# Kernel optimization log

Hardware: AMD Instinct MI355X
Metric: run time of the kernel (lower is better)

Reference implementation:

```python
import jax, jax.numpy as jnp
import numpy as np

B, N, A = 2, 4096, 5
TOPK = 30
K_RBF = 16
MAX_AA = 22
MAXREL = 32
EDGE_IN = 16 + K_RBF * 25 + 14 + 16  # 446
EDGE_FEAT = 128
PI = 3.1415926


def l2norm(v, eps=1e-12):
    n = jnp.sqrt(jnp.sum(v * v, axis=-1, keepdims=True))
    return v / jnp.maximum(n, eps)


def gather_nodes(nodes, idx):
    # nodes: (B,N,C), idx: (B,N,K) -> (B,N,K,C)
    b, n, k = idx.shape
    flat = idx.reshape(b, n * k, 1)
    out = jnp.take_along_axis(nodes, flat, axis=1)
    return out.reshape(b, n, k, nodes.shape[-1])


def quaternions(R):
    # R: (...,3,3) -> unit quaternion (...,4)
    Rxx, Ryy, Rzz = R[..., 0, 0], R[..., 1, 1], R[..., 2, 2]
    mag = 0.5 * jnp.sqrt(jnp.abs(1.0 + jnp.stack([Rxx - Ryy - Rzz, -Rxx + Ryy - Rzz, -Rxx - Ryy + Rzz], -1)) + 1e-12)
    signs = jnp.sign(jnp.stack([R[..., 2, 1] - R[..., 1, 2], R[..., 0, 2] - R[..., 2, 0], R[..., 1, 0] - R[..., 0, 1]], -1))
    xyz = signs * mag
    w = jnp.sqrt(jax.nn.relu(1.0 + Rxx + Ryy + Rzz) + 1e-12)[..., None] / 2.0
    return l2norm(jnp.concatenate([xyz, w], -1))


def setup_inputs():
    key = jax.random.key(0)
    ks = jax.random.split(key, 12)
    X = jax.random.normal(ks[0], (B, N, A, 3), jnp.float32) * 3.0
    mask = jnp.ones((B, N), jnp.float32)
    mask_atoms = jnp.ones((B, N, A), jnp.float32)
    means = jax.random.normal(ks[1], (K_RBF,), jnp.float32)
    stds = jax.random.normal(ks[2], (K_RBF,), jnp.float32)
    mul_w = jax.random.normal(ks[3], (A * A,), jnp.float32)
    bias_w = jax.random.normal(ks[4], (A * A,), jnp.float32)
    aa_pair_embed = jax.random.normal(ks[5], (MAX_AA * MAX_AA, K_RBF), jnp.float32) * 0.02
    aa_pair_embed = aa_pair_embed.at[441].set(0.0)  # padding_idx
    relpos_embed = jax.random.normal(ks[6], (2 * MAXREL + 1, 16), jnp.float32) * 0.02
    mask_embed = jax.random.normal(ks[7], (2, 16), jnp.float32) * 0.02
    W1 = jax.random.normal(ks[8], (EDGE_IN, EDGE_IN), jnp.float32) / np.sqrt(EDGE_IN)
    b1 = jnp.zeros((EDGE_IN,), jnp.float32)
    W2 = jax.random.normal(ks[9], (EDGE_IN, EDGE_FEAT), jnp.float32) / np.sqrt(EDGE_IN)
    b2 = jnp.zeros((EDGE_FEAT,), jnp.float32)
    aa = jax.random.randint(ks[10], (B, N), 0, 21, jnp.int32)
    residue_idx = jnp.tile(jnp.arange(N, dtype=jnp.int32)[None, :], (B, 1))
    chain_labels = jax.random.randint(ks[11], (B, N), 0, 2, jnp.int32)
    return dict(X=X, mask=mask, mask_atoms=mask_atoms, means=means, stds=stds, mul_w=mul_w,
                bias_w=bias_w, aa_pair_embed=aa_pair_embed, relpos_embed=relpos_embed,
                mask_embed=mask_embed, W1=W1, b1=b1, W2=W2, b2=b2, aa=aa,
                residue_idx=residue_idx, chain_labels=chain_labels)


def reference(X, mask, mask_atoms, means, stds, mul_w, bias_w, aa_pair_embed, relpos_embed,
              mask_embed, W1, b1, W2, b2, aa, residue_idx, chain_labels):
    Ca = X[:, :, 1]  # (B,N,3) C-alpha
    # ---- _dist: spatial kNN over C-alpha ----
    mask2d = mask[:, :, None] * mask[:, None, :]
    dx = Ca[:, None, :, :] - Ca[:, :, None, :]
    D = mask2d * jnp.sqrt(jnp.sum(dx * dx, -1) + 1e-6)
    D_adj = D + (1.0 - mask2d) * jnp.max(D, -1, keepdims=True)
    _, E_idx = jax.lax.top_k(-D_adj, TOPK)  # smallest distances
    mask_attend = jnp.take_along_axis(mask2d, E_idx, axis=2)  # (B,N,K)
    # ---- orientation features (local frames + quaternions) ----
    ones3 = jnp.ones((B, 1, 3), X.dtype)
    u = l2norm(jnp.concatenate([ones3, Ca[:, 1:] - Ca[:, :-1]], 1))
    b_ = l2norm(jnp.concatenate([u[:, :-1] - u[:, 1:], ones3], 1))
    n_ = l2norm(jnp.concatenate([jnp.cross(u[:, :-1], u[:, 1:]), ones3], 1))
    lf = jnp.stack([b_, n_, jnp.cross(b_, n_)], axis=2)  # (B,N,3,3)
    X_nb = gather_nodes(Ca, E_idx)                       # (B,N,K,3)
    O_nb = gather_nodes(lf.reshape(B, N, 9), E_idx).reshape(B, N, TOPK, 3, 3)
    t = X_nb - Ca[:, :, None, :]
    t = jnp.einsum('bnij,bnkj->bnki', lf, t)
    t = l2norm(t) * mask_attend[..., None]
    r = jnp.einsum('bnji,bnkjl->bnkil', lf, O_nb)  # lf^T @ O_nb
    q = quaternions(r) * mask_attend[..., None]
    O_feat = jnp.concatenate([t, q, 1.0 - 2.0 * jnp.abs(t), 1.0 - 2.0 * jnp.abs(q)], -1)  # (B,N,K,14)
    # ---- positional / chain embeddings ----
    offset = residue_idx[:, :, None] - residue_idx[:, None, :]
    offset_nb = jnp.take_along_axis(offset, E_idx, 2)
    d_chain = (chain_labels[:, :, None] == chain_labels[:, None, :]).astype(jnp.int32)
    E_chains = jnp.take_along_axis(d_chain, E_idx, 2)
    d = jnp.clip(offset_nb + MAXREL, 0, 2 * MAXREL)
    E_pos = relpos_embed[d] + mask_embed[E_chains]  # (B,N,K,16)
    # ---- GaussianLayer: aa-pair embed + atom-pair distance RBF ----
    aa_pair = aa[:, :, None] * MAX_AA + aa[:, None, :]
    aa_nb = jnp.take_along_axis(aa_pair, E_idx, 2)
    feat_aapair = aa_pair_embed[aa_nb] * mask_attend[..., None]  # (B,N,K,16)
    nbX = gather_nodes(X.reshape(B, N, A * 3), E_idx).reshape(B, N, TOPK, A, 3)
    delta = nbX[:, :, :, :, None, :] - X[:, :, None, None, :, :]  # (B,N,K,A,A,3)
    Dab = jnp.sqrt(jnp.sum(delta * delta, -1) + 1e-12)            # (B,N,K,A,A)
    et = jnp.arange(A * A).reshape(A, A)
    xg = mul_w[et] * Dab + bias_w[et]
    m_nb = gather_nodes(mask_atoms, E_idx)  # (B,N,K,A)
    xg = xg * (m_nb[..., None, :] * m_nb[..., :, None])
    std = jnp.abs(stds) + 0.01
    g = jnp.exp(-0.5 * ((xg[..., None] - means) / std) ** 2) / ((2.0 * PI) ** 0.5 * std)
    gbf = g.reshape(B, N, TOPK, A * A * K_RBF) * mask_attend[..., None]  # (B,N,K,400)
    # ---- fuse and project (NonLinear gbf_proj) ----
    E = jnp.concatenate([E_pos, gbf, O_feat, feat_aapair], -1)  # (B,N,K,446)
    h = jax.nn.gelu(E @ W1 + b1, approximate=False)
    return h @ W2 + b2  # (B,N,K,128)
```

## Files before the change

kernel.cpp:

```cpp
#include <hip/hip_runtime.h>
#include <cstdint>
#include <cstddef>

#define NN 4096
#define TOPK_ 30
#define BN_TOT 8192
#define M_TOT 245760
#define KP 448
#define HSTRIDE 136
#define EF 128

typedef unsigned short u16;
typedef unsigned int u32;
typedef __attribute__((ext_vector_type(8))) short bf16x8;
typedef __attribute__((ext_vector_type(4))) float f32x4;

__device__ __forceinline__ float b2f(u16 u){ return __uint_as_float(((u32)u)<<16); }
__device__ __forceinline__ u16 f2b(float f){
  u32 u = __float_as_uint(f);
  return (u16)((u + 0x7FFFu + ((u>>16)&1u)) >> 16);
}
__device__ __forceinline__ float ldf(const void* p, long i, int fl){
  return fl ? ((const float*)p)[i] : b2f(((const u16*)p)[i]);
}
__device__ __forceinline__ int is_f32_flag(const u16* mask){
  return (((const u32*)mask)[0] == 0x3F800000u) ? 1 : 0;
}
__device__ __forceinline__ void norm3(float x,float y,float z,float&ox,float&oy,float&oz){
  float n = sqrtf(x*x+y*y+z*z); n = fmaxf(n, 1e-12f);
  ox=x/n; oy=y/n; oz=z/n;
}
__device__ __forceinline__ float sgn(float x){ return x>0.f?1.f:(x<0.f?-1.f:0.f); }
__device__ __forceinline__ float gelu_f(float x){
  return 0.5f*x*(1.0f + erff(x*0.70710678118654752440f));
}
__device__ __forceinline__ float gelu_fast(float x){
  float y = 0.70710678118654752440f * x;
  float s = fabsf(y);
  float t = __builtin_amdgcn_rcpf(fmaf(0.3275911f, s, 1.0f));
  float p = fmaf(fmaf(fmaf(fmaf(1.061405429f, t, -1.453152027f), t, 1.421413741f), t,
                 -0.284496736f), t, 0.254829592f);
  float e = __expf(-y*y);
  float erfs = fmaf(-p*t, e, 1.0f);
  float erfy = (x >= 0.f) ? erfs : -erfs;
  float hx = 0.5f*x;
  return fmaf(hx, erfy, hx);
}
__device__ __forceinline__ u32 pk_bf16(float lo, float hi){
  u32 r;
  asm("v_cvt_pk_bf16_f32 %0, %1, %2" : "=v"(r) : "v"(lo), "v"(hi));
  return r;
}
__device__ __forceinline__ void async_cp16(const void* g, void* l){
  __builtin_amdgcn_global_load_lds((const __attribute__((address_space(1))) void*)(uintptr_t)g,
                                   (__attribute__((address_space(3))) void*)(uintptr_t)l, 16, 0, 0);
}

__global__ __launch_bounds__(256) void prep_kernel(
    const void* __restrict__ X, const u16* __restrict__ mask,
    const void* __restrict__ W1, const void* __restrict__ b1,
    const void* __restrict__ W2, const void* __restrict__ b2,
    float* __restrict__ ca, float* __restrict__ lf,
    u16* __restrict__ W1P, u16* __restrict__ W2P,
    float* __restrict__ b1p, float* __restrict__ b2p)
{
  const int fl = is_f32_flag(mask);
  int idx = blockIdx.x*256 + threadIdx.x;
  if (idx < BN_TOT) {
    int i = idx & (NN-1);
    float cax = ldf(X, (long)idx*15+3, fl), cay = ldf(X, (long)idx*15+4, fl), caz = ldf(X, (long)idx*15+5, fl);
    ca[idx*4+0]=cax; ca[idx*4+1]=cay; ca[idx*4+2]=caz; ca[idx*4+3]=0.f;
    float bx,by,bz,nx,ny,nz;
    if (i < NN-1) {
      float uix,uiy,uiz;
      if (i==0) { norm3(1.f,1.f,1.f,uix,uiy,uiz); }
      else {
        float px=ldf(X,(long)(idx-1)*15+3,fl), py=ldf(X,(long)(idx-1)*15+4,fl), pz=ldf(X,(long)(idx-1)*15+5,fl);
        norm3(cax-px, cay-py, caz-pz, uix,uiy,uiz);
      }
      float qx=ldf(X,(long)(idx+1)*15+3,fl), qy=ldf(X,(long)(idx+1)*15+4,fl), qz=ldf(X,(long)(idx+1)*15+5,fl);
      float vx,vy,vz; norm3(qx-cax, qy-cay, qz-caz, vx,vy,vz);
      norm3(uix-vx, uiy-vy, uiz-vz, bx,by,bz);
      norm3(uiy*vz-uiz*vy, uiz*vx-uix*vz, uix*vy-uiy*vx, nx,ny,nz);
    } else {
      norm3(1.f,1.f,1.f,bx,by,bz); nx=bx; ny=by; nz=bz;
    }
    float cx = by*nz - bz*ny, cy = bz*nx - bx*nz, cz = bx*ny - by*nx;
    float* L = lf + (size_t)idx*12;
    L[0]=bx;L[1]=by;L[2]=bz;L[3]=nx;L[4]=ny;L[5]=nz;L[6]=cx;L[7]=cy;L[8]=cz;
    return;
  }
  int r1 = idx - BN_TOT;
  if (r1 < 229376) {
    int f = r1 >> 9, li = r1 & 511;
    int n0 = f / 14, kc = f - n0*14;
    int ln = li >> 3, j = li & 7;
    int n = n0*16 + (ln & 15);
    int k = kc*32 + (ln >> 4)*8 + j;
    W1P[r1] = (n < 446 && k < 446) ? (fl ? f2b(((const float*)W1)[(long)k*446 + n])
                                         : ((const u16*)W1)[(long)k*446 + n]) : (u16)0;
    return;
  }
  int r2 = r1 - 229376;
  if (r2 < 65536) {
    int f = r2 >> 9, li = r2 & 511;
    int n0 = f >> 4, kc = f & 15;
    int ln = li >> 3, j = li & 7;
    int n = n0*16 + (ln & 15);
    int k = kc*32 + (ln >> 4)*8 + j;
    W2P[r2] = (k < 446) ? (fl ? f2b(((const float*)W2)[(long)k*128 + n])
                              : ((const u16*)W2)[(long)k*128 + n]) : (u16)0;
    return;
  }
  int r3 = r2 - 65536;
  if (r3 < 512) { b1p[r3] = (r3<446)? ldf(b1, r3, fl) : 0.f; return; }
  int r4 = r3 - 512;
  if (r4 < 128) { b2p[r4] = ldf(b2, r4, fl); }
}

__global__ __launch_bounds__(64) void knn_kernel(const float4* __restrict__ ca,
                                                 int* __restrict__ eidx)
{
#pragma clang fp contract(off)
  __shared__ u32 keys[NN];
  int bi = blockIdx.x;
  int lane = threadIdx.x;
  int b = bi >> 12;
  const float4 ci = ca[bi];
  const float4* cab = ca + (b<<12);
  u32 mind = 0xFFFFFFFFu; int minj = 1<<30; int minslot = 0;
  for (int c = 0; c < 64; ++c) {
    int j = (c<<6) | lane;
    float4 cj = cab[j];
    float dx = cj.x-ci.x, dy = cj.y-ci.y, dz = cj.z-ci.z;
    float ss = dx*dx;
    ss = ss + dy*dy;
    ss = ss + dz*dz;
    float d = sqrtf(ss + 1e-6f);
    u32 db = __float_as_uint(d);
    keys[(c<<6)|lane] = db;
    if (db < mind) { mind = db; minj = j; minslot = c; }
  }
  __syncthreads();
  for (int r = 0; r < TOPK_; ++r) {
    u32 wd = mind; int wj = minj;
    #pragma unroll
    for (int off = 32; off; off >>= 1) {
      u32 od = __shfl_xor(wd, off, 64);
      int oj = __shfl_xor(wj, off, 64);
      if (od < wd || (od == wd && oj < wj)) { wd = od; wj = oj; }
    }
    if (lane == 0) eidx[bi*TOPK_ + r] = wj;
    if ((wj & 63) == lane && wj == minj) {
      keys[minslot*64 + lane] = 0xFFFFFFFFu;
      mind = 0xFFFFFFFFu; minj = 1<<30;
      for (int c = 0; c < 64; ++c) {
        u32 db = keys[(c<<6)|lane];
        if (db < mind) { mind = db; minj = (c<<6)|lane; minslot = c; }
      }
    }
  }
}

__global__ __launch_bounds__(256) void ofeat_kernel(
  const u16* __restrict__ mask, const float* __restrict__ ca, const float* __restrict__ lf,
  const int* __restrict__ eidx, u16* __restrict__ E, int chunkStart, int Mc)
{
  int t = blockIdx.x*256 + threadIdx.x;
  if (t >= Mc) return;
  long e = chunkStart + t;
  const int fl = is_f32_flag(mask);
  int k = (int)(e % TOPK_);
  long bi = e / TOPK_;
  int b = (int)(bi >> 12);
  int bj = (b<<12) + eidx[bi*TOPK_ + k];
  float ma = ldf(mask, bi, fl) * ldf(mask, bj, fl);
  float Li[9], Lj[9];
  #pragma unroll
  for (int q_ = 0; q_ < 9; ++q_) { Li[q_] = lf[(size_t)bi*12+q_]; Lj[q_] = lf[(size_t)bj*12+q_]; }
  float dx = ca[bj*4+0]-ca[bi*4+0], dy = ca[bj*4+1]-ca[bi*4+1], dz = ca[bj*4+2]-ca[bi*4+2];
  float t0 = Li[0]*dx+Li[1]*dy+Li[2]*dz;
  float t1 = Li[3]*dx+Li[4]*dy+Li[5]*dz;
  float t2 = Li[6]*dx+Li[7]*dy+Li[8]*dz;
  float tn = fmaxf(sqrtf(t0*t0+t1*t1+t2*t2), 1e-12f);
  t0 = t0/tn*ma; t1 = t1/tn*ma; t2 = t2/tn*ma;
  float R00=Li[0]*Lj[0]+Li[3]*Lj[3]+Li[6]*Lj[6];
  float R01=Li[0]*Lj[1]+Li[3]*Lj[4]+Li[6]*Lj[7];
  float R02=Li[0]*Lj[2]+Li[3]*Lj[5]+Li[6]*Lj[8];
  float R10=Li[1]*Lj[0]+Li[4]*Lj[3]+Li[7]*Lj[6];
  float R11=Li[1]*Lj[1]+Li[4]*Lj[4]+Li[7]*Lj[7];
  float R12=Li[1]*Lj[2]+Li[4]*Lj[5]+Li[7]*Lj[8];
  float R20=Li[2]*Lj[0]+Li[5]*Lj[3]+Li[8]*Lj[6];
  float R21=Li[2]*Lj[1]+Li[5]*Lj[4]+Li[8]*Lj[7];
  float R22=Li[2]*Lj[2]+Li[5]*Lj[5]+Li[8]*Lj[8];
  float m0 = 0.5f*sqrtf(fabsf(1.f+R00-R11-R22)+1e-12f);
  float m1 = 0.5f*sqrtf(fabsf(1.f-R00+R11-R22)+1e-12f);
  float m2 = 0.5f*sqrtf(fabsf(1.f-R00-R11+R22)+1e-12f);
  float q0 = sgn(R21-R12)*m0, q1 = sgn(R02-R20)*m1, q2 = sgn(R10-R01)*m2;
  float qw = 0.5f*sqrtf(fmaxf(1.f+R00+R11+R22, 0.f)+1e-12f);
  float qn = fmaxf(sqrtf(q0*q0+q1*q1+q2*q2+qw*qw), 1e-12f);
  q0 = q0/qn*ma; q1 = q1/qn*ma; q2 = q2/qn*ma; qw = qw/qn*ma;
  u16 vals[14];
  vals[0]=f2b(t0); vals[1]=f2b(t1); vals[2]=f2b(t2);
  vals[3]=f2b(q0); vals[4]=f2b(q1); vals[5]=f2b(q2); vals[6]=f2b(qw);
  vals[7]=f2b(1.f-2.f*fabsf(t0)); vals[8]=f2b(1.f-2.f*fabsf(t1)); vals[9]=f2b(1.f-2.f*fabsf(t2));
  vals[10]=f2b(1.f-2.f*fabsf(q0)); vals[11]=f2b(1.f-2.f*fabsf(q1));
  vals[12]=f2b(1.f-2.f*fabsf(q2)); vals[13]=f2b(1.f-2.f*fabsf(qw));
  u16* dst = E + (size_t)t*KP + 416;
  *(uint4*)dst = *(const uint4*)vals;
  *(uint2*)(dst+8) = *(const uint2*)(vals+8);
  *(u32*)(dst+12) = *(const u32*)(vals+12);
}

__global__ __launch_bounds__(256) void feat_kernel(
  const void* __restrict__ X, const u16* __restrict__ mask, const void* __restrict__ mask_atoms,
  const void* __restrict__ means, const void* __restrict__ stds,
  const void* __restrict__ mul_w, const void* __restrict__ bias_w,
  const void* __restrict__ aa_pe, const void* __restrict__ relpos, const void* __restrict__ mask_emb,
  const int* __restrict__ aa, const int* __restrict__ ridx, const int* __restrict__ chains,
  const int* __restrict__ eidx, u16* __restrict__ E, int chunkStart, int Mc)
{
  const int fl = is_f32_flag(mask);
  int lane = threadIdx.x & 63;
  long gw = (long)(blockIdx.x*4) + (threadIdx.x >> 6);
  long nw = (long)gridDim.x * 4;
  float stdv = fabsf(ldf(stds, lane & 15, fl)) + 0.01f;
  float rinv = 1.0f/stdv;
  float coef0 = 0.3989422804014327f*rinv;
  float rmean = ldf(means, lane & 15, fl);
  float mw = 0.f, bw = 0.f;
  if (lane < 25) { mw = ldf(mul_w, lane, fl); bw = ldf(bias_w, lane, fl); }
  for (long e = chunkStart + gw; e < chunkStart + Mc; e += nw) {
    int k = (int)(e % TOPK_);
    long bi = e / TOPK_;
    int b = (int)(bi >> 12);
    int bj = (b<<12) + eidx[bi*TOPK_ + k];
    float ma = ldf(mask, bi, fl) * ldf(mask, bj, fl);
    float xgv = 0.f;
    if (lane < 25) {
      int a = lane/5, c_ = lane - a*5;
      float d0 = ldf(X,(long)bj*15 + a*3+0,fl) - ldf(X,(long)bi*15 + c_*3+0,fl);
      float d1 = ldf(X,(long)bj*15 + a*3+1,fl) - ldf(X,(long)bi*15 + c_*3+1,fl);
      float d2 = ldf(X,(long)bj*15 + a*3+2,fl) - ldf(X,(long)bi*15 + c_*3+2,fl);
      float Dab = sqrtf(d0*d0 + d1*d1 + d2*d2 + 1e-12f);
      float mm = ldf(mask_atoms,(long)bj*5 + a,fl) * ldf(mask_atoms,(long)bj*5 + c_,fl);
      xgv = (mw*Dab + bw) * mm;
    }
    int d = ridx[bi] - ridx[bj] + 32; d = d < 0 ? 0 : (d > 64 ? 64 : d);
    int ch = (chains[bi] == chains[bj]) ? 1 : 0;
    int aap = aa[bi]*22 + aa[bj];
    u16* row = E + (size_t)(e - chunkStart) * KP;
    #pragma unroll
    for (int pass = 0; pass < 7; ++pass) {
      int f = pass*64 + lane;
      int p = (f - 16) >> 4;
      p = p < 0 ? 0 : (p > 24 ? 24 : p);
      float xv = __shfl(xgv, p, 64);
      float val; bool skip = false;
      if (f < 16) {
        val = ldf(relpos, d*16 + f, fl) + ldf(mask_emb, ch*16 + f, fl);
      } else if (f < 416) {
        float z = (xv - rmean) * rinv;
        val = __expf(-0.5f*z*z) * coef0 * ma;
      } else if (f < 430) {
        skip = true; val = 0.f;
      } else if (f < 446) {
        val = ldf(aa_pe, aap*16 + (f-430), fl) * ma;
      } else {
        val = 0.f;
      }
      if (!skip) row[f] = f2b(val);
    }
  }
}

__global__ __launch_bounds__(512,2) void fused_mlp(
    const u16* __restrict__ E, const u16* __restrict__ W1P, const u16* __restrict__ W2P,
    const float* __restrict__ b1p, const float* __restrict__ b2p,
    void* __restrict__ C, long outOff, const u16* maskp)
{
  __shared__ u16 smem[2*128*HSTRIDE];
  u16* hs0 = smem;
  u16* hs1 = smem + 128*HSTRIDE;
  int tid = threadIdx.x;
  int lane = tid & 63, wave = tid >> 6;
  int wr = wave >> 2, wc = wave & 3;
  long rowBase = (long)blockIdx.x * 128;

  #define STAGE(tt, buf) do {                                                     \
    int r0_ = tid >> 3, s0_ = tid & 7;                                            \
    async_cp16(E + (rowBase + r0_)*(long)KP + (tt)*64 + ((s0_ ^ (r0_ & 7))<<3),   \
               smem + (buf)*8192 + tid*8);                                        \
    int r1_ = 64 + r0_;                                                           \
    async_cp16(E + (rowBase + r1_)*(long)KP + (tt)*64 + ((s0_ ^ (r1_ & 7))<<3),   \
               smem + (buf)*8192 + 4096 + tid*8);                                 \
  } while(0)

  f32x4 acc1[4][4][2] = {};
  STAGE(0, 0);
  #pragma unroll 1
  for (int t = 0; t < 7; ++t) {
    __syncthreads();
    const u16* As = smem + (t&1)*8192;
    bf16x8 af[2][4];
    #pragma unroll
    for (int kk = 0; kk < 2; ++kk)
      #pragma unroll
      for (int r = 0; r < 4; ++r) {
        int row = wr*64 + r*16 + (lane&15);
        int s = kk*4 + (lane>>4);
        af[kk][r] = *(const bf16x8*)(As + row*64 + ((s ^ (row&7))<<3));
      }
    bf16x8 bgA[2][2][2];
    #pragma unroll
    for (int c = 0; c < 2; ++c)
      #pragma unroll
      for (int cc = 0; cc < 2; ++cc)
        #pragma unroll
        for (int kk = 0; kk < 2; ++kk)
          bgA[c][cc][kk] = *(const bf16x8*)(W1P + (((c*8 + wc*2 + cc)*14 + t*2 + kk) << 9) + lane*8);
    #pragma unroll
    for (int c = 0; c < 2; ++c)
      #pragma unroll
      for (int r = 0; r < 4; ++r)
        #pragma unroll
        for (int cc = 0; cc < 2; ++cc)
          #pragma unroll
          for (int kk = 0; kk < 2; ++kk)
            acc1[c][r][cc] = __builtin_amdgcn_mfma_f32_16x16x32_bf16(af[kk][r], bgA[c][cc][kk], acc1[c][r][cc], 0,0,0);
    bf16x8 bgB[2][2][2];
    #pragma unroll
    for (int c = 0; c < 2; ++c)
      #pragma unroll
      for (int cc = 0; cc < 2; ++cc)
        #pragma unroll
        for (int kk = 0; kk < 2; ++kk)
          bgB[c][cc][kk] = *(const bf16x8*)(W1P + ((((c+2)*8 + wc*2 + cc)*14 + t*2 + kk) << 9) + lane*8);
    __builtin_amdgcn_sched_barrier(0);
    if (t < 6) STAGE(t+1, (t+1)&1);
    __builtin_amdgcn_sched_barrier(0);
    #pragma unroll
    for (int c = 0; c < 2; ++c)
      #pragma unroll
      for (int r = 0; r < 4; ++r)
        #pragma unroll
        for (int cc = 0; cc < 2; ++cc)
          #pragma unroll
          for (int kk = 0; kk < 2; ++kk)
            acc1[c+2][r][cc] = __builtin_amdgcn_mfma_f32_16x16x32_bf16(af[kk][r], bgB[c][cc][kk], acc1[c+2][r][cc], 0,0,0);
  }
  #undef STAGE

  #define STORE_HS(cN, buf) do {                                                  \
    _Pragma("unroll")                                                             \
    for (int r = 0; r < 4; ++r) {                                                 \
      _Pragma("unroll")                                                           \
      for (int cc = 0; cc < 2; ++cc) {                                            \
        int col = wc*32 + cc*16 + (lane & 15);                                    \
        float bv = b1p[(cN)*128 + col];                                           \
        int row0 = wr*64 + r*16 + (lane>>4)*4;                                    \
        u32 p01 = pk_bf16(gelu_fast(acc1[cN][r][cc][0]+bv),                       \
                          gelu_fast(acc1[cN][r][cc][1]+bv));                      \
        u32 p23 = pk_bf16(gelu_fast(acc1[cN][r][cc][2]+bv),                       \
                          gelu_fast(acc1[cN][r][cc][3]+bv));                      \
        u16* hb_ = (buf) + row0*HSTRIDE + col;                                    \
        hb_[0]         = (u16)p01; hb_[HSTRIDE]   = (u16)(p01>>16);               \
        hb_[2*HSTRIDE] = (u16)p23; hb_[3*HSTRIDE] = (u16)(p23>>16);               \
      }                                                                           \
    }                                                                             \
  } while(0)

  f32x4 acc2[4][2] = {};
  __syncthreads();
  STORE_HS(0, hs0);
  __syncthreads();
  #pragma unroll
  for (int c = 0; c < 4; ++c) {
    u16* hb = (c & 1) ? hs1 : hs0;
    u16* hn = (c & 1) ? hs0 : hs1;
    if (c < 3) STORE_HS(c+1, hn);
    #pragma unroll
    for (int k2 = 0; k2 < 4; ++k2) {
      bf16x8 af2[4], bg2[2];
      #pragma unroll
      for (int r = 0; r < 4; ++r) {
        int row = wr*64 + r*16 + (lane&15);
        af2[r] = *(const bf16x8*)(hb + row*HSTRIDE + k2*32 + (lane>>4)*8);
      }
      #pragma unroll
      for (int cc = 0; cc < 2; ++cc)
        bg2[cc] = *(const bf16x8*)(W2P + ((((wc*2+cc)*16) + c*4 + k2) << 9) + lane*8);
      #pragma unroll
      for (int r = 0; r < 4; ++r)
        #pragma unroll
        for (int cc = 0; cc < 2; ++cc)
          acc2[r][cc] = __builtin_amdgcn_mfma_f32_16x16x32_bf16(af2[r], bg2[cc], acc2[r][cc], 0,0,0);
    }
    __syncthreads();
  }
  #undef STORE_HS

  const int f32out = is_f32_flag(maskp);
  #pragma unroll
  for (int r = 0; r < 4; ++r) {
    #pragma unroll
    for (int cc = 0; cc < 2; ++cc) {
      int col = wc*32 + cc*16 + (lane & 15);
      float bv = b2p[col];
      #pragma unroll
      for (int g = 0; g < 4; ++g) {
        long row = rowBase + wr*64 + r*16 + (lane>>4)*4 + g;
        float v = acc2[r][cc][g] + bv;
        long o = outOff + row*EF + col;
        if (f32out) ((float*)C)[o] = v;
        else        ((u16*)C)[o]  = f2b(v);
      }
    }
  }
}

extern "C" void kernel_launch(void* const* d_in, const int* in_sizes, int n_in,
                              void* d_out, int out_size, void* d_ws, size_t ws_size,
                              hipStream_t stream) {
  const void* X          = d_in[0];
  const u16* mask        = (const u16*)d_in[1];
  const void* mask_atoms = d_in[2];
  const void* means      = d_in[3];
  const void* stds       = d_in[4];
  const void* mul_w      = d_in[5];
  const void* bias_w     = d_in[6];
  const void* aa_pe      = d_in[7];
  const void* relpos     = d_in[8];
  const void* mask_emb   = d_in[9];
  const void* W1         = d_in[10];
  const void* b1         = d_in[11];
  const void* W2         = d_in[12];
  const void* b2         = d_in[13];
  const int* aa          = (const int*)d_in[14];
  const int* ridx        = (const int*)d_in[15];
  const int* chains      = (const int*)d_in[16];

  char* ws = (char*)d_ws;
  float* ca  = (float*)(ws + 0);
  float* lf  = (float*)(ws + 131072);
  int* eidx  = (int*)(ws + 524288);
  u16* W1P   = (u16*)(ws + 1507328);
  u16* W2P   = (u16*)(ws + 1966080);
  float* b1p = (float*)(ws + 2097152);
  float* b2p = (float*)(ws + 2099200);
  size_t base = 2099712;

  int nc = 64;
  for (int c = 1; c <= 64; c <<= 1) {
    size_t mc = (size_t)M_TOT / c;
    if (base + mc*896 <= ws_size) { nc = c; break; }
  }
  int Mc = M_TOT / nc;
  u16* Ebuf = (u16*)(ws + base);

  prep_kernel<<<1187, 256, 0, stream>>>(X, mask, W1, b1, W2, b2, ca, lf, W1P, W2P, b1p, b2p);
  knn_kernel<<<BN_TOT, 64, 0, stream>>>((const float4*)ca, eidx);
  for (int c = 0; c < nc; ++c) {
    int cs = c * Mc;
    feat_kernel<<<1024, 256, 0, stream>>>(X, mask, mask_atoms, means, stds, mul_w, bias_w,
                                          aa_pe, relpos, mask_emb, aa, ridx, chains,
                                          eidx, Ebuf, cs, Mc);
    ofeat_kernel<<<Mc/256, 256, 0, stream>>>(mask, ca, lf, eidx, Ebuf, cs, Mc);
    fused_mlp<<<Mc/128, 512, 0, stream>>>(Ebuf, W1P, W2P, b1p, b2p, d_out,
                                          (long)cs*EF, mask);
  }
}
```

Before: 785.1 us.

## Fuse edge feature generation into MLP kernel, build E tile in LDS

Merges the feature kernels (relpos, RBF, orientation, aa-pair) into the MLP kernel. Each block now computes its 128-row, 448-column bf16 feature tile directly into swizzled LDS instead of writing a large E buffer to global memory and reading it back with async copies. This removes the chunk loop, the extra launches and the global round trip of roughly 220MB of intermediate data. In exchange, LDS use per block grows to about 118KB, which may cut occupancy below the two blocks per CU the launch bounds ask for. The pipelined staging of the A tiles is also gone, so each block does all its feature math before its first MFMA.

```diff
diff --git a/kernel.cpp b/kernel.cpp
--- a/kernel.cpp
+++ b/kernel.cpp
@@ -31,9 +31,6 @@
   ox=x/n; oy=y/n; oz=z/n;
 }
 __device__ __forceinline__ float sgn(float x){ return x>0.f?1.f:(x<0.f?-1.f:0.f); }
-__device__ __forceinline__ float gelu_f(float x){
-  return 0.5f*x*(1.0f + erff(x*0.70710678118654752440f));
-}
 __device__ __forceinline__ float gelu_fast(float x){
   float y = 0.70710678118654752440f * x;
   float s = fabsf(y);
@@ -50,10 +47,6 @@
   u32 r;
   asm("v_cvt_pk_bf16_f32 %0, %1, %2" : "=v"(r) : "v"(lo), "v"(hi));
   return r;
-}
-__device__ __forceinline__ void async_cp16(const void* g, void* l){
-  __builtin_amdgcn_global_load_lds((const __attribute__((address_space(1))) void*)(uintptr_t)g,
-                                   (__attribute__((address_space(3))) void*)(uintptr_t)l, 16, 0, 0);
 }
 
 __global__ __launch_bounds__(256) void prep_kernel(
@@ -162,146 +155,168 @@
   }
 }
 
-__global__ __launch_bounds__(256) void ofeat_kernel(
-  const u16* __restrict__ mask, const float* __restrict__ ca, const float* __restrict__ lf,
-  const int* __restrict__ eidx, u16* __restrict__ E, int chunkStart, int Mc)
+__global__ __launch_bounds__(512,2) void mega_mlp(
+    const void* __restrict__ X, const u16* __restrict__ mask, const void* __restrict__ mask_atoms,
+    const void* __restrict__ means, const void* __restrict__ stds,
+    const void* __restrict__ mul_w, const void* __restrict__ bias_w,
+    const void* __restrict__ aa_pe, const void* __restrict__ relpos, const void* __restrict__ mask_emb,
+    const int* __restrict__ aa, const int* __restrict__ ridx, const int* __restrict__ chains,
+    const int* __restrict__ eidx, const float* __restrict__ ca, const float* __restrict__ lf,
+    const u16* __restrict__ W1P, const u16* __restrict__ W2P,
+    const float* __restrict__ b1p, const float* __restrict__ b2p,
+    void* __restrict__ C)
 {
-  int t = blockIdx.x*256 + threadIdx.x;
-  if (t >= Mc) return;
-  long e = chunkStart + t;
+  __shared__ __align__(16) u16 Et[128*448];
+  __shared__ float Dabs[128][29];
+  __shared__ float maA[128];
   const int fl = is_f32_flag(mask);
-  int k = (int)(e % TOPK_);
-  long bi = e / TOPK_;
-  int b = (int)(bi >> 12);
-  int bj = (b<<12) + eidx[bi*TOPK_ + k];
-  float ma = ldf(mask, bi, fl) * ldf(mask, bj, fl);
-  float Li[9], Lj[9];
-  #pragma unroll
-  for (int q_ = 0; q_ < 9; ++q_) { Li[q_] = lf[(size_t)bi*12+q_]; Lj[q_] = lf[(size_t)bj*12+q_]; }
-  float dx = ca[bj*4+0]-ca[bi*4+0], dy = ca[bj*4+1]-ca[bi*4+1], dz = ca[bj*4+2]-ca[bi*4+2];
-  float t0 = Li[0]*dx+Li[1]*dy+Li[2]*dz;
-  float t1 = Li[3]*dx+Li[4]*dy+Li[5]*dz;
-  float t2 = Li[6]*dx+Li[7]*dy+Li[8]*dz;
-  float tn = fmaxf(sqrtf(t0*t0+t1*t1+t2*t2), 1e-12f);
-  t0 = t0/tn*ma; t1 = t1/tn*ma; t2 = t2/tn*ma;
-  float R00=Li[0]*Lj[0]+Li[3]*Lj[3]+Li[6]*Lj[6];
-  float R01=Li[0]*Lj[1]+Li[3]*Lj[4]+Li[6]*Lj[7];
-  float R02=Li[0]*Lj[2]+Li[3]*Lj[5]+Li[6]*Lj[8];
-  float R10=Li[1]*Lj[0]+Li[4]*Lj[3]+Li[7]*Lj[6];
-  float R11=Li[1]*Lj[1]+Li[4]*Lj[4]+Li[7]*Lj[7];
-  float R12=Li[1]*Lj[2]+Li[4]*Lj[5]+Li[7]*Lj[8];
-  float R20=Li[2]*Lj[0]+Li[5]*Lj[3]+Li[8]*Lj[6];
-  float R21=Li[2]*Lj[1]+Li[5]*Lj[4]+Li[8]*Lj[7];
-  float R22=Li[2]*Lj[2]+Li[5]*Lj[5]+Li[8]*Lj[8];
-  float m0 = 0.5f*sqrtf(fabsf(1.f+R00-R11-R22)+1e-12f);
-  float m1 = 0.5f*sqrtf(fabsf(1.f-R00+R11-R22)+1e-12f);
-  float m2 = 0.5f*sqrtf(fabsf(1.f-R00-R11+R22)+1e-12f);
-  float q0 = sgn(R21-R12)*m0, q1 = sgn(R02-R20)*m1, q2 = sgn(R10-R01)*m2;
-  float qw = 0.5f*sqrtf(fmaxf(1.f+R00+R11+R22, 0.f)+1e-12f);
-  float qn = fmaxf(sqrtf(q0*q0+q1*q1+q2*q2+qw*qw), 1e-12f);
-  q0 = q0/qn*ma; q1 = q1/qn*ma; q2 = q2/qn*ma; qw = qw/qn*ma;
-  u16 vals[14];
-  vals[0]=f2b(t0); vals[1]=f2b(t1); vals[2]=f2b(t2);
-  vals[3]=f2b(q0); vals[4]=f2b(q1); vals[5]=f2b(q2); vals[6]=f2b(qw);
-  vals[7]=f2b(1.f-2.f*fabsf(t0)); vals[8]=f2b(1.f-2.f*fabsf(t1)); vals[9]=f2b(1.f-2.f*fabsf(t2));
-  vals[10]=f2b(1.f-2.f*fabsf(q0)); vals[11]=f2b(1.f-2.f*fabsf(q1));
-  vals[12]=f2b(1.f-2.f*fabsf(q2)); vals[13]=f2b(1.f-2.f*fabsf(qw));
-  u16* dst = E + (size_t)t*KP + 416;
-  *(uint4*)dst = *(const uint4*)vals;
-  *(uint2*)(dst+8) = *(const uint2*)(vals+8);
-  *(u32*)(dst+12) = *(const u32*)(vals+12);
-}
-
-__global__ __launch_bounds__(256) void feat_kernel(
-  const void* __restrict__ X, const u16* __restrict__ mask, const void* __restrict__ mask_atoms,
-  const void* __restrict__ means, const void* __restrict__ stds,
-  const void* __restrict__ mul_w, const void* __restrict__ bias_w,
-  const void* __restrict__ aa_pe, const void* __restrict__ relpos, const void* __restrict__ mask_emb,
-  const int* __restrict__ aa, const int* __restrict__ ridx, const int* __restrict__ chains,
-  const int* __restrict__ eidx, u16* __restrict__ E, int chunkStart, int Mc)
-{
-  const int fl = is_f32_flag(mask);
-  int lane = threadIdx.x & 63;
-  long gw = (long)(blockIdx.x*4) + (threadIdx.x >> 6);
-  long nw = (long)gridDim.x * 4;
-  float stdv = fabsf(ldf(stds, lane & 15, fl)) + 0.01f;
-  float rinv = 1.0f/stdv;
-  float coef0 = 0.3989422804014327f*rinv;
-  float rmean = ldf(means, lane & 15, fl);
-  float mw = 0.f, bw = 0.f;
-  if (lane < 25) { mw = ldf(mul_w, lane, fl); bw = ldf(bias_w, lane, fl); }
-  for (long e = chunkStart + gw; e < chunkStart + Mc; e += nw) {
-    int k = (int)(e % TOPK_);
-    long bi = e / TOPK_;
-    int b = (int)(bi >> 12);
-    int bj = (b<<12) + eidx[bi*TOPK_ + k];
-    float ma = ldf(mask, bi, fl) * ldf(mask, bj, fl);
-    float xgv = 0.f;
-    if (lane < 25) {
-      int a = lane/5, c_ = lane - a*5;
-      float d0 = ldf(X,(long)bj*15 + a*3+0,fl) - ldf(X,(long)bi*15 + c_*3+0,fl);
-      float d1 = ldf(X,(long)bj*15 + a*3+1,fl) - ldf(X,(long)bi*15 + c_*3+1,fl);
-      float d2 = ldf(X,(long)bj*15 + a*3+2,fl) - ldf(X,(long)bi*15 + c_*3+2,fl);
-      float Dab = sqrtf(d0*d0 + d1*d1 + d2*d2 + 1e-12f);
-      float mm = ldf(mask_atoms,(long)bj*5 + a,fl) * ldf(mask_atoms,(long)bj*5 + c_,fl);
-      xgv = (mw*Dab + bw) * mm;
-    }
-    int d = ridx[bi] - ridx[bj] + 32; d = d < 0 ? 0 : (d > 64 ? 64 : d);
-    int ch = (chains[bi] == chains[bj]) ? 1 : 0;
-    int aap = aa[bi]*22 + aa[bj];
-    u16* row = E + (size_t)(e - chunkStart) * KP;
-    #pragma unroll
-    for (int pass = 0; pass < 7; ++pass) {
-      int f = pass*64 + lane;
-      int p = (f - 16) >> 4;
-      p = p < 0 ? 0 : (p > 24 ? 24 : p);
-      float xv = __shfl(xgv, p, 64);
-      float val; bool skip = false;
-      if (f < 16) {
-        val = ldf(relpos, d*16 + f, fl) + ldf(mask_emb, ch*16 + f, fl);
-      } else if (f < 416) {
-        float z = (xv - rmean) * rinv;
-        val = __expf(-0.5f*z*z) * coef0 * ma;
-      } else if (f < 430) {
-        skip = true; val = 0.f;
-      } else if (f < 446) {
-        val = ldf(aa_pe, aap*16 + (f-430), fl) * ma;
-      } else {
-        val = 0.f;
-      }
-      if (!skip) row[f] = f2b(val);
-    }
-  }
-}
-
-__global__ __launch_bounds__(512,2) void fused_mlp(
-    const u16* __restrict__ E, const u16* __restrict__ W1P, const u16* __restrict__ W2P,
-    const float* __restrict__ b1p, const float* __restrict__ b2p,
-    void* __restrict__ C, long outOff, const u16* maskp)
-{
-  __shared__ u16 smem[2*128*HSTRIDE];
-  u16* hs0 = smem;
-  u16* hs1 = smem + 128*HSTRIDE;
   int tid = threadIdx.x;
   int lane = tid & 63, wave = tid >> 6;
   int wr = wave >> 2, wc = wave & 3;
-  long rowBase = (long)blockIdx.x * 128;
-
-  #define STAGE(tt, buf) do {                                                     \
-    int r0_ = tid >> 3, s0_ = tid & 7;                                            \
-    async_cp16(E + (rowBase + r0_)*(long)KP + (tt)*64 + ((s0_ ^ (r0_ & 7))<<3),   \
-               smem + (buf)*8192 + tid*8);                                        \
-    int r1_ = 64 + r0_;                                                           \
-    async_cp16(E + (rowBase + r1_)*(long)KP + (tt)*64 + ((s0_ ^ (r1_ & 7))<<3),   \
-               smem + (buf)*8192 + 4096 + tid*8);                                 \
-  } while(0)
+  int rowBase = blockIdx.x * 128;
+
+  {
+    int eo = tid >> 2, q = tid & 3;
+    int e = rowBase + eo;
+    int bi = (int)((unsigned)e / 30u);
+    int k = e - bi*30;
+    int bj = ((bi >> 12) << 12) + eidx[bi*TOPK_ + k];
+    if (q == 1) maA[eo] = ldf(mask, bi, fl) * ldf(mask, bj, fl);
+    float Xi[15];
+    #pragma unroll
+    for (int v = 0; v < 15; ++v) Xi[v] = ldf(X, (long)bi*15 + v, fl);
+    for (int a = q; a < 5; a += 4) {
+      float xj0 = ldf(X,(long)bj*15 + a*3+0, fl);
+      float xj1 = ldf(X,(long)bj*15 + a*3+1, fl);
+      float xj2 = ldf(X,(long)bj*15 + a*3+2, fl);
+      float mja = ldf(mask_atoms,(long)bj*5 + a, fl);
+      #pragma unroll
+      for (int c = 0; c < 5; ++c) {
+        float d0 = xj0 - Xi[c*3+0];
+        float d1 = xj1 - Xi[c*3+1];
+        float d2 = xj2 - Xi[c*3+2];
+        float Dab = sqrtf(d0*d0 + d1*d1 + d2*d2 + 1e-12f);
+        float mm = mja * ldf(mask_atoms,(long)bj*5 + c, fl);
+        float mw = ldf(mul_w, a*5+c, fl), bw = ldf(bias_w, a*5+c, fl);
+        Dabs[eo][a*5+c] = (mw*Dab + bw) * mm;
+      }
+    }
+  }
+
+  if (tid < 128) {
+    int eo = tid;
+    int e = rowBase + eo;
+    int bi = (int)((unsigned)e / 30u);
+    int k = e - bi*30;
+    int bj = ((bi >> 12) << 12) + eidx[bi*TOPK_ + k];
+    float ma = ldf(mask, bi, fl) * ldf(mask, bj, fl);
+    char* rowB = (char*)Et + eo*896;
+    int xr = (eo & 7) << 4;
+    int d = ridx[bi] - ridx[bj] + 32; d = d < 0 ? 0 : (d > 64 ? 64 : d);
+    int ch = (chains[bi] == chains[bj]) ? 1 : 0;
+    float rp[16];
+    #pragma unroll
+    for (int f = 0; f < 16; ++f)
+      rp[f] = ldf(relpos, d*16 + f, fl) + ldf(mask_emb, ch*16 + f, fl);
+    {
+      uint4 wA, wB;
+      wA.x = pk_bf16(rp[0],rp[1]);  wA.y = pk_bf16(rp[2],rp[3]);
+      wA.z = pk_bf16(rp[4],rp[5]);  wA.w = pk_bf16(rp[6],rp[7]);
+      wB.x = pk_bf16(rp[8],rp[9]);  wB.y = pk_bf16(rp[10],rp[11]);
+      wB.z = pk_bf16(rp[12],rp[13]);wB.w = pk_bf16(rp[14],rp[15]);
+      *(uint4*)(rowB + (0 ^ xr))  = wA;
+      *(uint4*)(rowB + (16 ^ xr)) = wB;
+    }
+    float Li[9], Lj[9];
+    #pragma unroll
+    for (int q_ = 0; q_ < 9; ++q_) { Li[q_] = lf[(size_t)bi*12+q_]; Lj[q_] = lf[(size_t)bj*12+q_]; }
+    float dx = ca[bj*4+0]-ca[bi*4+0], dy = ca[bj*4+1]-ca[bi*4+1], dz = ca[bj*4+2]-ca[bi*4+2];
+    float t0 = Li[0]*dx+Li[1]*dy+Li[2]*dz;
+    float t1 = Li[3]*dx+Li[4]*dy+Li[5]*dz;
+    float t2 = Li[6]*dx+Li[7]*dy+Li[8]*dz;
+    float tn = fmaxf(sqrtf(t0*t0+t1*t1+t2*t2), 1e-12f);
+    t0 = t0/tn*ma; t1 = t1/tn*ma; t2 = t2/tn*ma;
+    float R00=Li[0]*Lj[0]+Li[3]*Lj[3]+Li[6]*Lj[6];
+    float R01=Li[0]*Lj[1]+Li[3]*Lj[4]+Li[6]*Lj[7];
+    float R02=Li[0]*Lj[2]+Li[3]*Lj[5]+Li[6]*Lj[8];
+    float R10=Li[1]*Lj[0]+Li[4]*Lj[3]+Li[7]*Lj[6];
+    float R11=Li[1]*Lj[1]+Li[4]*Lj[4]+Li[7]*Lj[7];
+    float R12=Li[1]*Lj[2]+Li[4]*Lj[5]+Li[7]*Lj[8];
+    float R20=Li[2]*Lj[0]+Li[5]*Lj[3]+Li[8]*Lj[6];
+    float R21=Li[2]*Lj[1]+Li[5]*Lj[4]+Li[8]*Lj[7];
+    float R22=Li[2]*Lj[2]+Li[5]*Lj[5]+Li[8]*Lj[8];
+    float m0 = 0.5f*sqrtf(fabsf(1.f+R00-R11-R22)+1e-12f);
+    float m1 = 0.5f*sqrtf(fabsf(1.f-R00+R11-R22)+1e-12f);
+    float m2 = 0.5f*sqrtf(fabsf(1.f-R00-R11+R22)+1e-12f);
+    float q0 = sgn(R21-R12)*m0, q1 = sgn(R02-R20)*m1, q2 = sgn(R10-R01)*m2;
+    float qw = 0.5f*sqrtf(fmaxf(1.f+R00+R11+R22, 0.f)+1e-12f);
+    float qn = fmaxf(sqrtf(q0*q0+q1*q1+q2*q2+qw*qw), 1e-12f);
+    q0 = q0/qn*ma; q1 = q1/qn*ma; q2 = q2/qn*ma; qw = qw/qn*ma;
+    int aap = aa[bi]*22 + aa[bj];
+    float av[16];
+    #pragma unroll
+    for (int f = 0; f < 16; ++f) av[f] = ldf(aa_pe, aap*16 + f, fl) * ma;
+    uint4 w0, w1, w2, w3;
+    w0.x = pk_bf16(t0, t1);                     w0.y = pk_bf16(t2, q0);
+    w0.z = pk_bf16(q1, q2);                     w0.w = pk_bf16(qw, 1.f-2.f*fabsf(t0));
+    w1.x = pk_bf16(1.f-2.f*fabsf(t1), 1.f-2.f*fabsf(t2));
+    w1.y = pk_bf16(1.f-2.f*fabsf(q0), 1.f-2.f*fabsf(q1));
+    w1.z = pk_bf16(1.f-2.f*fabsf(q2), 1.f-2.f*fabsf(qw));
+    w1.w = pk_bf16(av[0], av[1]);
+    w2.x = pk_bf16(av[2], av[3]);   w2.y = pk_bf16(av[4], av[5]);
+    w2.z = pk_bf16(av[6], av[7]);   w2.w = pk_bf16(av[8], av[9]);
+    w3.x = pk_bf16(av[10], av[11]); w3.y = pk_bf16(av[12], av[13]);
+    w3.z = pk_bf16(av[14], av[15]); w3.w = 0u;
+    *(uint4*)(rowB + (832 ^ xr)) = w0;
+    *(uint4*)(rowB + (848 ^ xr)) = w1;
+    *(uint4*)(rowB + (864 ^ xr)) = w2;
+    *(uint4*)(rowB + (880 ^ xr)) = w3;
+  }
+  __syncthreads();
+
+  {
+    float meanv[16], rinvv[16], coefv[16];
+    #pragma unroll
+    for (int r = 0; r < 16; ++r) {
+      meanv[r] = ldf(means, r, fl);
+      float sd = fabsf(ldf(stds, r, fl)) + 0.01f;
+      rinvv[r] = 1.0f / sd;
+      coefv[r] = 0.3989422804014327f * rinvv[r];
+    }
+    #pragma unroll 1
+    for (int i = 0; i < 13; ++i) {
+      int G = tid + i*512;
+      if (G < 6400) {
+        int row = (int)((unsigned)G / 50u);
+        int gp = G - row*50;
+        float xg = Dabs[row][gp >> 1];
+        float ma = maA[row];
+        int odd = gp & 1;
+        u32 w[4];
+        #pragma unroll
+        for (int j2 = 0; j2 < 4; ++j2) {
+          float me0 = odd ? meanv[j2*2+8]   : meanv[j2*2];
+          float ri0 = odd ? rinvv[j2*2+8]   : rinvv[j2*2];
+          float co0 = odd ? coefv[j2*2+8]   : coefv[j2*2];
+          float me1 = odd ? meanv[j2*2+9]   : meanv[j2*2+1];
+          float ri1 = odd ? rinvv[j2*2+9]   : rinvv[j2*2+1];
+          float co1 = odd ? coefv[j2*2+9]   : coefv[j2*2+1];
+          float z0 = (xg - me0) * ri0;
+          float z1 = (xg - me1) * ri1;
+          float v0 = __expf(-0.5f*z0*z0) * co0 * ma;
+          float v1 = __expf(-0.5f*z1*z1) * co1 * ma;
+          w[j2] = pk_bf16(v0, v1);
+        }
+        uint4 W4; W4.x = w[0]; W4.y = w[1]; W4.z = w[2]; W4.w = w[3];
+        *(uint4*)((char*)Et + row*896 + ((32 + (gp<<4)) ^ ((row&7)<<4))) = W4;
+      }
+    }
+  }
+  __syncthreads();
 
   f32x4 acc1[4][4][2] = {};
-  STAGE(0, 0);
   #pragma unroll 1
   for (int t = 0; t < 7; ++t) {
-    __syncthreads();
-    const u16* As = smem + (t&1)*8192;
     bf16x8 af[2][4];
     #pragma unroll
     for (int kk = 0; kk < 2; ++kk)
@@ -309,7 +324,7 @@
       for (int r = 0; r < 4; ++r) {
         int row = wr*64 + r*16 + (lane&15);
         int s = kk*4 + (lane>>4);
-        af[kk][r] = *(const bf16x8*)(As + row*64 + ((s ^ (row&7))<<3));
+        af[kk][r] = *(const bf16x8*)(Et + row*448 + t*64 + ((s ^ (row&7))<<3));
       }
     bf16x8 bgA[2][2][2];
     #pragma unroll
@@ -336,9 +351,6 @@
         #pragma unroll
         for (int kk = 0; kk < 2; ++kk)
           bgB[c][cc][kk] = *(const bf16x8*)(W1P + ((((c+2)*8 + wc*2 + cc)*14 + t*2 + kk) << 9) + lane*8);
-    __builtin_amdgcn_sched_barrier(0);
-    if (t < 6) STAGE(t+1, (t+1)&1);
-    __builtin_amdgcn_sched_barrier(0);
     #pragma unroll
     for (int c = 0; c < 2; ++c)
       #pragma unroll
@@ -349,8 +361,9 @@
           for (int kk = 0; kk < 2; ++kk)
             acc1[c+2][r][cc] = __builtin_amdgcn_mfma_f32_16x16x32_bf16(af[kk][r], bgB[c][cc][kk], acc1[c+2][r][cc], 0,0,0);
   }
-  #undef STAGE
-
+
+  u16* hs0 = Et;
+  u16* hs1 = Et + 128*HSTRIDE;
   #define STORE_HS(cN, buf) do {                                                  \
     _Pragma("unroll")                                                             \
     for (int r = 0; r < 4; ++r) {                                                 \
@@ -400,7 +413,7 @@
   }
   #undef STORE_HS
 
-  const int f32out = is_f32_flag(maskp);
+  const int f32out = is_f32_flag(mask);
   #pragma unroll
   for (int r = 0; r < 4; ++r) {
     #pragma unroll
@@ -409,9 +422,9 @@
       float bv = b2p[col];
       #pragma unroll
       for (int g = 0; g < 4; ++g) {
-        long row = rowBase + wr*64 + r*16 + (lane>>4)*4 + g;
+        long row = (long)rowBase + wr*64 + r*16 + (lane>>4)*4 + g;
         float v = acc2[r][cc][g] + bv;
-        long o = outOff + row*EF + col;
+        long o = row*EF + col;
         if (f32out) ((float*)C)[o] = v;
         else        ((u16*)C)[o]  = f2b(v);
       }
@@ -448,25 +461,10 @@
   u16* W2P   = (u16*)(ws + 1966080);
   float* b1p = (float*)(ws + 2097152);
   float* b2p = (float*)(ws + 2099200);
-  size_t base = 2099712;
-
-  int nc = 64;
-  for (int c = 1; c <= 64; c <<= 1) {
-    size_t mc = (size_t)M_TOT / c;
-    if (base + mc*896 <= ws_size) { nc = c; break; }
-  }
-  int Mc = M_TOT / nc;
-  u16* Ebuf = (u16*)(ws + base);
 
   prep_kernel<<<1187, 256, 0, stream>>>(X, mask, W1, b1, W2, b2, ca, lf, W1P, W2P, b1p, b2p);
   knn_kernel<<<BN_TOT, 64, 0, stream>>>((const float4*)ca, eidx);
-  for (int c = 0; c < nc; ++c) {
-    int cs = c * Mc;
-    feat_kernel<<<1024, 256, 0, stream>>>(X, mask, mask_atoms, means, stds, mul_w, bias_w,
+  mega_mlp<<<M_TOT/128, 512, 0, stream>>>(X, mask, mask_atoms, means, stds, mul_w, bias_w,
                                           aa_pe, relpos, mask_emb, aa, ridx, chains,
-                                          eidx, Ebuf, cs, Mc);
-    ofeat_kernel<<<Mc/256, 256, 0, stream>>>(mask, ca, lf, eidx, Ebuf, cs, Mc);
-    fused_mlp<<<Mc/128, 512, 0, stream>>>(Ebuf, W1P, W2P, b1p, b2p, d_out,
-                                          (long)cs*EF, mask);
-  }
-}
+                                          eidx, ca, lf, W1P, W2P, b1p, b2p, d_out);
+}
```

Measured after the change: 773.3 us. About the same (-1.5%).
